# Performance work log

Measured on AMD Instinct MI355X. Metric: run time of the kernel, lower is better.

Reference implementation:

```python
import jax, jax.numpy as jnp
import numpy as np

NEG_SLOPE = 0.2  # PyG GATConv default leaky_relu slope

def gat_conv(x, src, dst, W, a_src, a_dst, bias, N):
    # Linear transform
    h = x @ W                      # [N, D]
    # Per-node attention logits (heads=1)
    al_src = h @ a_src             # [N]
    al_dst = h @ a_dst             # [N]
    e = jax.nn.leaky_relu(al_src[src] + al_dst[dst], NEG_SLOPE)  # [E]
    # Segment softmax over incoming edges of each destination node
    m = jax.ops.segment_max(e, dst, num_segments=N)
    ex = jnp.exp(e - m[dst])
    denom = jax.ops.segment_sum(ex, dst, num_segments=N)
    alpha = ex / denom[dst]        # [E]
    # Weighted scatter-aggregate of source features
    out = jax.ops.segment_sum(h[src] * alpha[:, None], dst, num_segments=N)
    return out + bias

def setup_inputs() -> dict:
    key = jax.random.key(0)
    ks = jax.random.split(key, 10)
    N, E, F_in, H, O = 50000, 800000, 128, 64, 64
    x = jax.random.normal(ks[0], (N, F_in), dtype=jnp.float32)
    edge_index = jax.random.randint(ks[1], (2, E), 0, N, dtype=jnp.int32)
    s = lambda k, shp, fan: jax.random.normal(k, shp, dtype=jnp.float32) / np.sqrt(fan)
    return {
        'x': x, 'edge_index': edge_index,
        'W1': s(ks[2], (F_in, H), F_in), 'a_src1': s(ks[3], (H,), H), 'a_dst1': s(ks[4], (H,), H), 'b1': jnp.zeros((H,), jnp.float32),
        'W2': s(ks[5], (H, O), H), 'a_src2': s(ks[6], (O,), O), 'a_dst2': s(ks[7], (O,), O), 'b2': jnp.zeros((O,), jnp.float32),
    }

def reference(x, edge_index, W1, a_src1, a_dst1, b1, W2, a_src2, a_dst2, b2):
    N = x.shape[0]
    loops = jnp.arange(N, dtype=edge_index.dtype)  # PyG adds self-loops by default
    src = jnp.concatenate([edge_index[0], loops])
    dst = jnp.concatenate([edge_index[1], loops])
    h = gat_conv(x, src, dst, W1, a_src1, a_dst1, b1, N)
    h = jax.nn.relu(h)
    # dropout(p=0.6) is identity in eval mode
    out = gat_conv(h, src, dst, W2, a_src2, a_dst2, b2, N)
    return out
```

## Files before the change

kernel.cpp:

```cpp
#include <hip/hip_runtime.h>
#include <hip/hip_bf16.h>

#define DEV static __device__ __forceinline__

typedef short bf16x8 __attribute__((ext_vector_type(8)));
typedef float f32x4  __attribute__((ext_vector_type(4)));
typedef unsigned u32x4 __attribute__((ext_vector_type(4)));

union U4 { uint4 u; bf16x8 s; };

DEV float b2f(__hip_bfloat16 v) { return __bfloat162float(v); }
DEV float lrelu(float e) { return e > 0.f ? e : 0.2f * e; }

DEV unsigned short f2bu(float f) {
    __hip_bfloat16 b = __float2bfloat16(f);
    return *reinterpret_cast<unsigned short*>(&b);
}
DEV float bu2f(unsigned short u) { return __uint_as_float((unsigned)u << 16); }

DEV float loadF(const void* p, size_t i, int f32) {
    if (f32) return ((const float*)p)[i];
    return b2f(((const __hip_bfloat16*)p)[i]);
}

DEV uint4 pack8(const unsigned short* t) {
    uint4 v;
    v.x = (unsigned)t[0] | ((unsigned)t[1] << 16);
    v.y = (unsigned)t[2] | ((unsigned)t[3] << 16);
    v.z = (unsigned)t[4] | ((unsigned)t[5] << 16);
    v.w = (unsigned)t[6] | ((unsigned)t[7] << 16);
    return v;
}

DEV u32x4 pack8v(const unsigned short* t) {
    u32x4 v;
    v.x = (unsigned)t[0] | ((unsigned)t[1] << 16);
    v.y = (unsigned)t[2] | ((unsigned)t[3] << 16);
    v.z = (unsigned)t[4] | ((unsigned)t[5] << 16);
    v.w = (unsigned)t[6] | ((unsigned)t[7] << 16);
    return v;
}

DEV void edge_sd(int i, int E, const int* __restrict__ src, const int* __restrict__ dst,
                 int& s, int& d) {
    if (i < E) { s = src[i]; d = dst[i]; }
    else       { s = d = i - E; }
}

DEV int detect_wave(const void* p, int n, int lane) {
    const unsigned short* u16 = (const unsigned short*)p;
    bool insane = false;
#pragma unroll
    for (int r = 0; r < 4; ++r) {
        int idx = lane + r * 64;
        if (idx < n) {
            unsigned short u = u16[idx];
            unsigned e = (u >> 7) & 0xFFu;
            insane |= (e >= 0xC8u) || (e == 0u && (u & 0x7Fu) != 0u);
        }
    }
    return (__ballot(insane) != 0ull) ? 1 : 0;
}

#define G_BIN 128

__global__ __launch_bounds__(256) void k_fused1(
    const void* __restrict__ x, const void* __restrict__ W,
    const void* __restrict__ a_s, const void* __restrict__ a_d,
    __hip_bfloat16* __restrict__ h, float* __restrict__ als, float* __restrict__ ald,
    int N, int gb, int nx, int nW1,
    const int* __restrict__ src, const int* __restrict__ dst,
    int* __restrict__ hist, int E, int EA, int chunk,
    const void* a5, int n5, const void* a6, int n6, const void* a7, int n7,
    const void* a8, int n8, const void* a9, int n9,
    int* __restrict__ flags)
{
    const int tid = threadIdx.x;
    const int bid = blockIdx.x;

    if (bid >= gb) {
        if (bid == gb + G_BIN) {
            const void* ps[9] = {x, W, a_s, a_d, a5, a6, a7, a8, a9};
            const int   ns[9] = {nx, nW1, 64, 64, n5, n6, n7, n8, n9};
            const int w = tid >> 6, lane = tid & 63;
            for (int k = w; k < 9; k += 4) {
                int f = detect_wave(ps[k], ns[k], lane);
                if (lane == 0) flags[k] = f;
            }
            return;
        }
        __shared__ int cnt[256];
        cnt[tid] = 0;
        __syncthreads();
        const int cb = bid - gb;
        const int lo = cb * chunk;
        const int hi = min(lo + chunk, EA);
        for (int i = lo + tid; i < hi; i += 256) {
            int s, d; edge_sd(i, E, src, dst, s, d);
            atomicAdd(&cnt[d >> 8], 1);
        }
        __syncthreads();
        hist[cb * 256 + tid] = cnt[tid];
        return;
    }

    __shared__ __align__(16) unsigned short sMem[2 * 64 * 136];
    __shared__ float sAs[64], sAd[64];
    __shared__ int sFl[4];
    unsigned short* sA = sMem;
    unsigned short* sB = sMem + 64 * 136;
    float* sOut = (float*)sMem;

    {
        const void* ps4[4] = {x, W, a_s, a_d};
        const int   ns4[4] = {nx, nW1, 64, 64};
        const int w = tid >> 6, lane = tid & 63;
        int f = detect_wave(ps4[w], ns4[w], lane);
        if (lane == 0) sFl[w] = f;
    }
    __syncthreads();
    const int fx = sFl[0], fw = sFl[1];

    const int row0 = bid * 64;
    if (tid < 64) sAs[tid] = loadF(a_s, tid, sFl[2]);
    else if (tid < 128) sAd[tid - 64] = loadF(a_d, tid - 64, sFl[3]);

    if (!fx) {
        const uint4* xg = (const uint4*)x;
#pragma unroll
        for (int it = 0; it < 2; ++it) {
            int g = tid + it * 256;
            int r = g >> 4, c16 = g & 15;
            uint4 v = (row0 + r < N) ? xg[(size_t)(row0 + r) * 16 + c16]
                                     : make_uint4(0, 0, 0, 0);
            *(uint4*)(sA + r * 136 + c16 * 8) = v;
        }
    } else {
        for (int i = tid; i < 64 * 128; i += 256) {
            int r = i >> 7, k = i & 127;
            float v = (row0 + r < N) ? ((const float*)x)[(size_t)(row0 + r) * 128 + k] : 0.f;
            sA[r * 136 + k] = f2bu(v);
        }
    }
    if (!fw) {
        const unsigned short* Wg = (const unsigned short*)W;
        const int n = tid & 63;
        int k0 = (tid >> 6) * 8;
#pragma unroll
        for (int rep = 0; rep < 4; ++rep, k0 += 32) {
            unsigned short t[8];
#pragma unroll
            for (int j = 0; j < 8; ++j) t[j] = Wg[(size_t)(k0 + j) * 64 + n];
            *(uint4*)(sB + n * 136 + k0) = pack8(t);
        }
    } else {
        const float* Wg = (const float*)W;
        for (int i = tid; i < 128 * 64; i += 256) {
            int k = i >> 6, n = i & 63;
            sB[n * 136 + k] = f2bu(Wg[i]);
        }
    }
    __syncthreads();

    const int w = tid >> 6, lane = tid & 63;
    const int m0 = w * 16;
    const int qr = lane >> 4;
    const int lc = lane & 15;

    bf16x8 afrag[4];
#pragma unroll
    for (int c = 0; c < 4; ++c) {
        U4 u; u.u = *(const uint4*)(sA + (m0 + lc) * 136 + c * 32 + qr * 8);
        afrag[c] = u.s;
    }
    f32x4 accs[4];
#pragma unroll
    for (int nt = 0; nt < 4; ++nt) {
        f32x4 acc = {0.f, 0.f, 0.f, 0.f};
#pragma unroll
        for (int c = 0; c < 4; ++c) {
            U4 u; u.u = *(const uint4*)(sB + (nt * 16 + lc) * 136 + c * 32 + qr * 8);
            acc = __builtin_amdgcn_mfma_f32_16x16x32_bf16(afrag[c], u.s, acc, 0, 0, 0);
        }
        accs[nt] = acc;
    }
    __syncthreads();

#pragma unroll
    for (int nt = 0; nt < 4; ++nt)
#pragma unroll
        for (int reg = 0; reg < 4; ++reg)
            sOut[(m0 + qr * 4 + reg) * 68 + nt * 16 + lc] = accs[nt][reg];
    __syncthreads();

    {
        const int r = tid >> 2, seg = tid & 3;
        const int row = row0 + r;
        const float* po = sOut + r * 68 + seg * 16;
        float ps = 0.f, pd = 0.f;
        unsigned short ob[16];
#pragma unroll
        for (int i = 0; i < 16; ++i) {
            float v = po[i];
            ps = fmaf(v, sAs[seg * 16 + i], ps);
            pd = fmaf(v, sAd[seg * 16 + i], pd);
            ob[i] = f2bu(v);
        }
        if (row < N) {
            uint4* hp = (uint4*)((unsigned short*)h + (size_t)row * 64 + seg * 16);
            hp[0] = pack8(ob);
            hp[1] = pack8(ob + 8);
        }
        ps += __shfl_xor(ps, 1, 64); ps += __shfl_xor(ps, 2, 64);
        pd += __shfl_xor(pd, 1, 64); pd += __shfl_xor(pd, 2, 64);
        if (seg == 0 && row < N) { als[row] = ps; ald[row] = pd; }
    }
}

__global__ __launch_bounds__(G_BIN) void k_binB1(
    const int* __restrict__ hist, int* __restrict__ offs_rel,
    int* __restrict__ btot)
{
    __shared__ int sm[G_BIN];
    const int t = threadIdx.x;
    const int b = blockIdx.x;
    int v = hist[t * 256 + b];
    sm[t] = v;
    __syncthreads();
#pragma unroll
    for (int off = 1; off < G_BIN; off <<= 1) {
        int u = (t >= off) ? sm[t - off] : 0;
        __syncthreads();
        sm[t] += u;
        __syncthreads();
    }
    offs_rel[t * 256 + b] = sm[t] - v;
    if (t == G_BIN - 1) btot[b] = sm[t];
}

__global__ __launch_bounds__(256) void k_binC(
    const int* __restrict__ src, const int* __restrict__ dst,
    const int* __restrict__ offs_rel, const int* __restrict__ btot,
    unsigned* __restrict__ ebuf, int E, int EA, int chunk)
{
    __shared__ int sm[256];
    __shared__ int cur[256];
    const int tid = threadIdx.x;
    int v = btot[tid];
    sm[tid] = v;
    __syncthreads();
#pragma unroll
    for (int off = 1; off < 256; off <<= 1) {
        int t = (tid >= off) ? sm[tid - off] : 0;
        __syncthreads();
        sm[tid] += t;
        __syncthreads();
    }
    cur[tid] = (sm[tid] - v) + offs_rel[blockIdx.x * 256 + tid];
    __syncthreads();
    const int lo = blockIdx.x * chunk;
    const int hi = min(lo + chunk, EA);
    for (int i = lo + tid; i < hi; i += 256) {
        int s, d; edge_sd(i, E, src, dst, s, d);
        int pos = atomicAdd(&cur[d >> 8], 1);
        ebuf[pos] = ((unsigned)(d & 255) << 17) | (unsigned)s;
    }
}

__global__ __launch_bounds__(256) void k_binD(
    const unsigned* __restrict__ ebuf, const int* __restrict__ btot,
    int* __restrict__ row_ptr, int* __restrict__ col, int N)
{
    __shared__ int sm[256];
    __shared__ int cnt[256];
    __shared__ int pfx[256];
    const int tid = threadIdx.x;
    const int b = blockIdx.x;
    {
        int v = btot[tid];
        sm[tid] = v;
        __syncthreads();
#pragma unroll
        for (int off = 1; off < 256; off <<= 1) {
            int t = (tid >= off) ? sm[tid - off] : 0;
            __syncthreads();
            sm[tid] += t;
            __syncthreads();
        }
    }
    const int lo = (b == 0) ? 0 : sm[b - 1];
    const int hi = sm[b];
    cnt[tid] = 0;
    __syncthreads();
    for (int i = lo + tid; i < hi; i += 256)
        atomicAdd(&cnt[ebuf[i] >> 17], 1);
    __syncthreads();
    const int c = cnt[tid];
    pfx[tid] = c;
    __syncthreads();
#pragma unroll
    for (int off = 1; off < 256; off <<= 1) {
        int t = (tid >= off) ? pfx[tid - off] : 0;
        __syncthreads();
        pfx[tid] += t;
        __syncthreads();
    }
    const int excl = pfx[tid] - c;
    const int d = b * 256 + tid;
    if (d <= N) row_ptr[d] = lo + excl;
    __syncthreads();
    cnt[tid] = lo + excl;
    __syncthreads();
    for (int i = lo + tid; i < hi; i += 256) {
        unsigned v = ebuf[i];
        int pos = atomicAdd(&cnt[v >> 17], 1);
        col[pos] = (int)(v & 0x1FFFFu);
    }
}

__global__ __launch_bounds__(256) void k_gemm2(
    __hip_bfloat16* __restrict__ agg, const void* __restrict__ b1,
    const void* __restrict__ W, const void* __restrict__ a_s,
    const void* __restrict__ a_d, const int* __restrict__ flags,
    float* __restrict__ als, float* __restrict__ ald, int N)
{
    __shared__ __align__(16) unsigned short sMem[2 * 64 * 72];
    __shared__ float sAs[64], sAd[64], sBias[64];
    unsigned short* sA = sMem;
    unsigned short* sB = sMem + 64 * 72;
    float* sOut = (float*)sMem;

    const int tid = threadIdx.x;
    const int row0 = blockIdx.x * 64;
    const int fw = flags[5];

    if (tid < 64) sAs[tid] = loadF(a_s, tid, flags[6]);
    else if (tid < 128) sAd[tid - 64] = loadF(a_d, tid - 64, flags[7]);
    else if (tid < 192) sBias[tid - 128] = loadF(b1, tid - 128, flags[4]);
    __syncthreads();

    {
        const uint4* ag = (const uint4*)agg;
#pragma unroll
        for (int it = 0; it < 2; ++it) {
            int g = tid + it * 256;
            int r = g >> 3, c8 = g & 7;
            uint4 v = (row0 + r < N) ? ag[(size_t)(row0 + r) * 8 + c8]
                                     : make_uint4(0, 0, 0, 0);
            unsigned short in[8] = {
                (unsigned short)(v.x & 0xFFFF), (unsigned short)(v.x >> 16),
                (unsigned short)(v.y & 0xFFFF), (unsigned short)(v.y >> 16),
                (unsigned short)(v.z & 0xFFFF), (unsigned short)(v.z >> 16),
                (unsigned short)(v.w & 0xFFFF), (unsigned short)(v.w >> 16)};
            unsigned short ob[8];
#pragma unroll
            for (int j = 0; j < 8; ++j) {
                float t = bu2f(in[j]) + sBias[c8 * 8 + j];
                ob[j] = f2bu(t > 0.f ? t : 0.f);
            }
            *(uint4*)(sA + r * 72 + c8 * 8) = pack8(ob);
        }
    }
    if (!fw) {
        const unsigned short* Wg = (const unsigned short*)W;
        const int n = tid & 63;
        int k0 = (tid >> 6) * 8;
#pragma unroll
        for (int rep = 0; rep < 2; ++rep, k0 += 32) {
            unsigned short t[8];
#pragma unroll
            for (int j = 0; j < 8; ++j) t[j] = Wg[(size_t)(k0 + j) * 64 + n];
            *(uint4*)(sB + n * 72 + k0) = pack8(t);
        }
    } else {
        const float* Wg = (const float*)W;
        for (int i = tid; i < 64 * 64; i += 256) {
            int k = i >> 6, n = i & 63;
            sB[n * 72 + k] = f2bu(Wg[i]);
        }
    }
    __syncthreads();

    const int w = tid >> 6, lane = tid & 63;
    const int m0 = w * 16;
    const int qr = lane >> 4, lc = lane & 15;

    bf16x8 afrag[2];
#pragma unroll
    for (int c = 0; c < 2; ++c) {
        U4 u; u.u = *(const uint4*)(sA + (m0 + lc) * 72 + c * 32 + qr * 8);
        afrag[c] = u.s;
    }
    f32x4 accs[4];
#pragma unroll
    for (int nt = 0; nt < 4; ++nt) {
        f32x4 acc = {0.f, 0.f, 0.f, 0.f};
#pragma unroll
        for (int c = 0; c < 2; ++c) {
            U4 u; u.u = *(const uint4*)(sB + (nt * 16 + lc) * 72 + c * 32 + qr * 8);
            acc = __builtin_amdgcn_mfma_f32_16x16x32_bf16(afrag[c], u.s, acc, 0, 0, 0);
        }
        accs[nt] = acc;
    }
    __syncthreads();
#pragma unroll
    for (int nt = 0; nt < 4; ++nt)
#pragma unroll
        for (int reg = 0; reg < 4; ++reg)
            sOut[(m0 + qr * 4 + reg) * 68 + nt * 16 + lc] = accs[nt][reg];
    __syncthreads();

    {
        const int r = tid >> 2, seg = tid & 3;
        const int row = row0 + r;
        const float* po = sOut + r * 68 + seg * 16;
        float ps = 0.f, pd = 0.f;
        unsigned short ob[16];
#pragma unroll
        for (int i = 0; i < 16; ++i) {
            float v = po[i];
            ps = fmaf(v, sAs[seg * 16 + i], ps);
            pd = fmaf(v, sAd[seg * 16 + i], pd);
            ob[i] = f2bu(v);
        }
        if (row < N) {
            uint4* hp = (uint4*)((unsigned short*)agg + (size_t)row * 64 + seg * 16);
            hp[0] = pack8(ob);
            hp[1] = pack8(ob + 8);
        }
        ps += __shfl_xor(ps, 1, 64); ps += __shfl_xor(ps, 2, 64);
        pd += __shfl_xor(pd, 1, 64); pd += __shfl_xor(pd, 2, 64);
        if (seg == 0 && row < N) { als[row] = ps; ald[row] = pd; }
    }
}

__global__ __launch_bounds__(256) void k_gather(
    const int* __restrict__ row_ptr, const int* __restrict__ col,
    const float* __restrict__ als, const float* __restrict__ ald,
    const __hip_bfloat16* __restrict__ h,
    __hip_bfloat16* __restrict__ agg_out,
    void* __restrict__ final_out,
    const void* __restrict__ bias, const int* __restrict__ flags, int N)
{
    const int tid = threadIdx.x;
    const int lane = tid & 63;
    const int eg = lane >> 3, fg = lane & 7;
    const int wid = blockIdx.x * 4 + (tid >> 6);
    const int nw  = gridDim.x * 4;

    for (int d = wid; d < N; d += nw) {
        const float aldd = ald[d];
        const int beg = row_ptr[d], end = row_ptr[d + 1];
        float acc[8] = {0.f,0.f,0.f,0.f,0.f,0.f,0.f,0.f};
        float den = 0.f;
        for (int j = beg + eg; j < end; j += 8) {
            const int s = col[j];
            const float w = __expf(lrelu(als[s] + aldd));
            den += w;
            const uint4 hv = *reinterpret_cast<const uint4*>(h + (size_t)s * 64 + fg * 8);
            acc[0] = fmaf(w, __uint_as_float(hv.x << 16),          acc[0]);
            acc[1] = fmaf(w, __uint_as_float(hv.x & 0xFFFF0000u),  acc[1]);
            acc[2] = fmaf(w, __uint_as_float(hv.y << 16),          acc[2]);
            acc[3] = fmaf(w, __uint_as_float(hv.y & 0xFFFF0000u),  acc[3]);
            acc[4] = fmaf(w, __uint_as_float(hv.z << 16),          acc[4]);
            acc[5] = fmaf(w, __uint_as_float(hv.z & 0xFFFF0000u),  acc[5]);
            acc[6] = fmaf(w, __uint_as_float(hv.w << 16),          acc[6]);
            acc[7] = fmaf(w, __uint_as_float(hv.w & 0xFFFF0000u),  acc[7]);
        }
#pragma unroll
        for (int off = 8; off <= 32; off <<= 1) {
            den += __shfl_xor(den, off, 64);
#pragma unroll
            for (int k = 0; k < 8; ++k) acc[k] += __shfl_xor(acc[k], off, 64);
        }
        if (eg == 0) {
            const float inv = 1.f / den;
            if (final_out) {
                float vb[8];
#pragma unroll
                for (int k = 0; k < 8; ++k) vb[k] = acc[k] * inv + loadF(bias, fg * 8 + k, flags[8]);
                if (flags[0]) {
                    float* o = (float*)final_out + (size_t)d * 64 + fg * 8;
                    f32x4 o0 = {vb[0], vb[1], vb[2], vb[3]};
                    f32x4 o1 = {vb[4], vb[5], vb[6], vb[7]};
                    __builtin_nontemporal_store(o0, (f32x4*)o);
                    __builtin_nontemporal_store(o1, (f32x4*)(o + 4));
                } else {
                    unsigned short ob[8];
#pragma unroll
                    for (int k = 0; k < 8; ++k) ob[k] = f2bu(vb[k]);
                    __builtin_nontemporal_store(pack8v(ob),
                        reinterpret_cast<u32x4*>((__hip_bfloat16*)final_out + (size_t)d * 64 + fg * 8));
                }
            } else {
                unsigned short ob[8];
#pragma unroll
                for (int k = 0; k < 8; ++k) ob[k] = f2bu(acc[k] * inv);
                __builtin_nontemporal_store(pack8v(ob),
                    reinterpret_cast<u32x4*>(agg_out + (size_t)d * 64 + fg * 8));
            }
        }
    }
}

extern "C" void kernel_launch(void* const* d_in, const int* in_sizes, int n_in,
                              void* d_out, int out_size, void* d_ws, size_t ws_size,
                              hipStream_t stream)
{
    const void* x   = d_in[0];
    const int*  ei  = (const int*)d_in[1];
    const void* W1  = d_in[2];
    const void* as1 = d_in[3];
    const void* ad1 = d_in[4];
    const void* b1  = d_in[5];
    const void* W2  = d_in[6];
    const void* as2 = d_in[7];
    const void* ad2 = d_in[8];
    const void* b2  = d_in[9];

    const int N  = in_sizes[0] / 128;
    const int E  = in_sizes[1] / 2;
    const int EA = E + N;
    const int* src = ei;
    const int* dst = ei + E;

    uintptr_t base = (uintptr_t)d_ws;
    auto alloc = [&](size_t bytes) { uintptr_t p = base; base += (bytes + 63) & ~(size_t)63; return p; };
    int*      flags    = (int*)alloc(64 * 4);
    float*    als      = (float*)alloc((size_t)N * 4);
    float*    ald      = (float*)alloc((size_t)N * 4);
    int*      row_ptr  = (int*)alloc((size_t)(N + 1) * 4);
    int*      hist     = (int*)alloc((size_t)G_BIN * 256 * 4);
    int*      offs_rel = (int*)alloc((size_t)G_BIN * 256 * 4);
    int*      btot     = (int*)alloc(256 * 4);
    unsigned* ebuf     = (unsigned*)alloc((size_t)EA * 4);
    int*      col      = (int*)alloc((size_t)EA * 4);
    __hip_bfloat16* hbuf   = (__hip_bfloat16*)alloc((size_t)N * 64 * 2);
    __hip_bfloat16* aggbuf = (__hip_bfloat16*)alloc((size_t)N * 64 * 2);

    const int gatherb = 2048;
    const int gb  = (N + 63) / 64;
    const int NBK = (N + 255) / 256;
    const int chunk = (EA + G_BIN - 1) / G_BIN;

    k_fused1<<<gb + G_BIN + 1, 256, 0, stream>>>(
        x, W1, as1, ad1, hbuf, als, ald, N, gb, in_sizes[0], in_sizes[2],
        src, dst, hist, E, EA, chunk,
        b1, in_sizes[5], W2, in_sizes[6], as2, in_sizes[7], ad2, in_sizes[8],
        b2, in_sizes[9], flags);
    k_binB1<<<256, G_BIN, 0, stream>>>(hist, offs_rel, btot);
    k_binC<<<G_BIN, 256, 0, stream>>>(src, dst, offs_rel, btot, ebuf, E, EA, chunk);
    k_binD<<<NBK, 256, 0, stream>>>(ebuf, btot, row_ptr, col, N);

    k_gather<<<gatherb, 256, 0, stream>>>(row_ptr, col, als, ald, hbuf, aggbuf,
                                          nullptr, nullptr, flags, N);
    k_gemm2<<<gb, 256, 0, stream>>>(aggbuf, b1, W2, as2, ad2, flags, als, ald, N);
    k_gather<<<gatherb, 256, 0, stream>>>(row_ptr, col, als, ald, aggbuf, nullptr,
                                          d_out, b2, flags, N);
    (void)out_size; (void)ws_size; (void)n_in;
}
```

Baseline: 199.6 us.

## Fuse CSR build into first kernel with device-wide barriers; prefetch in gather

Moves the histogram, scan, scatter and per-bucket sort stages of the CSR construction into the first fused kernel. The first 256 blocks run them, separated by atomic-counter grid barriers, while the remaining blocks compute the GEMM. This removes three kernel launches and their serialization. The gather kernel now gives each wave a contiguous range of nodes, loads row_ptr and ald once per wave and broadcasts them with shuffles, and prefetches the next edge's column and logit. The grid barrier assumes all 256 CSR blocks are co-resident, which risks deadlock if they are not. It also adds a memset launch.

```diff
diff --git a/kernel.cpp b/kernel.cpp
--- a/kernel.cpp
+++ b/kernel.cpp
@@ -62,7 +62,19 @@
     return (__ballot(insane) != 0ull) ? 1 : 0;
 }
 
-#define G_BIN 128
+#define GCSR 256
+
+DEV void dev_barrier(int* ctr, int target) {
+    __syncthreads();
+    if (threadIdx.x == 0) {
+        __threadfence();
+        __hip_atomic_fetch_add(ctr, 1, __ATOMIC_ACQ_REL, __HIP_MEMORY_SCOPE_AGENT);
+        while (__hip_atomic_load(ctr, __ATOMIC_ACQUIRE, __HIP_MEMORY_SCOPE_AGENT) < target)
+            __builtin_amdgcn_s_sleep(8);
+        __threadfence();
+    }
+    __syncthreads();
+}
 
 __global__ __launch_bounds__(256) void k_fused1(
     const void* __restrict__ x, const void* __restrict__ W,
@@ -70,7 +82,9 @@
     __hip_bfloat16* __restrict__ h, float* __restrict__ als, float* __restrict__ ald,
     int N, int gb, int nx, int nW1,
     const int* __restrict__ src, const int* __restrict__ dst,
-    int* __restrict__ hist, int E, int EA, int chunk,
+    int* __restrict__ hist, int E, int EA, int chunk, int NBK,
+    unsigned* __restrict__ ebuf, int* __restrict__ col, int* __restrict__ row_ptr,
+    int* __restrict__ ctrs,
     const void* a5, int n5, const void* a6, int n6, const void* a7, int n7,
     const void* a8, int n8, const void* a9, int n9,
     int* __restrict__ flags)
@@ -78,35 +92,99 @@
     const int tid = threadIdx.x;
     const int bid = blockIdx.x;
 
-    if (bid >= gb) {
-        if (bid == gb + G_BIN) {
-            const void* ps[9] = {x, W, a_s, a_d, a5, a6, a7, a8, a9};
-            const int   ns[9] = {nx, nW1, 64, 64, n5, n6, n7, n8, n9};
-            const int w = tid >> 6, lane = tid & 63;
-            for (int k = w; k < 9; k += 4) {
-                int f = detect_wave(ps[k], ns[k], lane);
-                if (lane == 0) flags[k] = f;
-            }
-            return;
-        }
-        __shared__ int cnt[256];
-        cnt[tid] = 0;
-        __syncthreads();
-        const int cb = bid - gb;
-        const int lo = cb * chunk;
-        const int hi = min(lo + chunk, EA);
-        for (int i = lo + tid; i < hi; i += 256) {
-            int s, d; edge_sd(i, E, src, dst, s, d);
-            atomicAdd(&cnt[d >> 8], 1);
-        }
-        __syncthreads();
-        hist[cb * 256 + tid] = cnt[tid];
-        return;
-    }
-
     __shared__ __align__(16) unsigned short sMem[2 * 64 * 136];
     __shared__ float sAs[64], sAd[64];
     __shared__ int sFl[4];
+
+    if (bid < GCSR) {
+        int* p0 = (int*)sMem;
+        int* p1 = p0 + 256;
+        int* pE = p1 + 256;
+        int* pI = pE + 256;
+        const int cb = bid;
+        const int lo = cb * chunk;
+        const int hi = min(lo + chunk, EA);
+
+        p0[tid] = 0;
+        __syncthreads();
+        for (int i = lo + tid; i < hi; i += 256) {
+            int s, d; edge_sd(i, E, src, dst, s, d);
+            atomicAdd(&p0[d >> 8], 1);
+        }
+        __syncthreads();
+        hist[cb * 256 + tid] = p0[tid];
+        dev_barrier(ctrs + 0, GCSR);
+
+        int tot = 0, mine = 0;
+        for (int c = 0; c < GCSR; ++c) {
+            int v = hist[c * 256 + tid];
+            tot += v;
+            if (c < cb) mine += v;
+        }
+        p1[tid] = tot;
+        __syncthreads();
+#pragma unroll
+        for (int off = 1; off < 256; off <<= 1) {
+            int u = (tid >= off) ? p1[tid - off] : 0;
+            __syncthreads();
+            p1[tid] += u;
+            __syncthreads();
+        }
+        pI[tid] = p1[tid];
+        pE[tid] = p1[tid] - tot;
+        p0[tid] = pE[tid] + mine;
+        __syncthreads();
+        for (int i = lo + tid; i < hi; i += 256) {
+            int s, d; edge_sd(i, E, src, dst, s, d);
+            int pos = atomicAdd(&p0[d >> 8], 1);
+            ebuf[pos] = ((unsigned)(d & 255) << 17) | (unsigned)s;
+        }
+        dev_barrier(ctrs + 1, GCSR);
+
+        for (int b = cb; b < NBK; b += GCSR) {
+            const int blo = pE[b], bhi = pI[b];
+            p0[tid] = 0;
+            __syncthreads();
+            for (int i = blo + tid; i < bhi; i += 256)
+                atomicAdd(&p0[ebuf[i] >> 17], 1);
+            __syncthreads();
+            const int c = p0[tid];
+            p1[tid] = c;
+            __syncthreads();
+#pragma unroll
+            for (int off = 1; off < 256; off <<= 1) {
+                int u = (tid >= off) ? p1[tid - off] : 0;
+                __syncthreads();
+                p1[tid] += u;
+                __syncthreads();
+            }
+            const int excl = p1[tid] - c;
+            const int dd = b * 256 + tid;
+            if (dd <= N) row_ptr[dd] = blo + excl;
+            __syncthreads();
+            p0[tid] = blo + excl;
+            __syncthreads();
+            for (int i = blo + tid; i < bhi; i += 256) {
+                unsigned v = ebuf[i];
+                int pos = atomicAdd(&p0[v >> 17], 1);
+                col[pos] = (int)(v & 0x1FFFFu);
+            }
+            __syncthreads();
+        }
+        return;
+    }
+
+    if (bid == GCSR + gb) {
+        const void* ps[9] = {x, W, a_s, a_d, a5, a6, a7, a8, a9};
+        const int   ns[9] = {nx, nW1, 64, 64, n5, n6, n7, n8, n9};
+        const int w = tid >> 6, lane = tid & 63;
+        for (int k = w; k < 9; k += 4) {
+            int f = detect_wave(ps[k], ns[k], lane);
+            if (lane == 0) flags[k] = f;
+        }
+        return;
+    }
+
     unsigned short* sA = sMem;
     unsigned short* sB = sMem + 64 * 136;
     float* sOut = (float*)sMem;
@@ -121,7 +199,7 @@
     __syncthreads();
     const int fx = sFl[0], fw = sFl[1];
 
-    const int row0 = bid * 64;
+    const int row0 = (bid - GCSR) * 64;
     if (tid < 64) sAs[tid] = loadF(a_s, tid, sFl[2]);
     else if (tid < 128) sAd[tid - 64] = loadF(a_d, tid - 64, sFl[3]);
 
@@ -214,107 +292,6 @@
         ps += __shfl_xor(ps, 1, 64); ps += __shfl_xor(ps, 2, 64);
         pd += __shfl_xor(pd, 1, 64); pd += __shfl_xor(pd, 2, 64);
         if (seg == 0 && row < N) { als[row] = ps; ald[row] = pd; }
-    }
-}
-
-__global__ __launch_bounds__(G_BIN) void k_binB1(
-    const int* __restrict__ hist, int* __restrict__ offs_rel,
-    int* __restrict__ btot)
-{
-    __shared__ int sm[G_BIN];
-    const int t = threadIdx.x;
-    const int b = blockIdx.x;
-    int v = hist[t * 256 + b];
-    sm[t] = v;
-    __syncthreads();
-#pragma unroll
-    for (int off = 1; off < G_BIN; off <<= 1) {
-        int u = (t >= off) ? sm[t - off] : 0;
-        __syncthreads();
-        sm[t] += u;
-        __syncthreads();
-    }
-    offs_rel[t * 256 + b] = sm[t] - v;
-    if (t == G_BIN - 1) btot[b] = sm[t];
-}
-
-__global__ __launch_bounds__(256) void k_binC(
-    const int* __restrict__ src, const int* __restrict__ dst,
-    const int* __restrict__ offs_rel, const int* __restrict__ btot,
-    unsigned* __restrict__ ebuf, int E, int EA, int chunk)
-{
-    __shared__ int sm[256];
-    __shared__ int cur[256];
-    const int tid = threadIdx.x;
-    int v = btot[tid];
-    sm[tid] = v;
-    __syncthreads();
-#pragma unroll
-    for (int off = 1; off < 256; off <<= 1) {
-        int t = (tid >= off) ? sm[tid - off] : 0;
-        __syncthreads();
-        sm[tid] += t;
-        __syncthreads();
-    }
-    cur[tid] = (sm[tid] - v) + offs_rel[blockIdx.x * 256 + tid];
-    __syncthreads();
-    const int lo = blockIdx.x * chunk;
-    const int hi = min(lo + chunk, EA);
-    for (int i = lo + tid; i < hi; i += 256) {
-        int s, d; edge_sd(i, E, src, dst, s, d);
-        int pos = atomicAdd(&cur[d >> 8], 1);
-        ebuf[pos] = ((unsigned)(d & 255) << 17) | (unsigned)s;
-    }
-}
-
-__global__ __launch_bounds__(256) void k_binD(
-    const unsigned* __restrict__ ebuf, const int* __restrict__ btot,
-    int* __restrict__ row_ptr, int* __restrict__ col, int N)
-{
-    __shared__ int sm[256];
-    __shared__ int cnt[256];
-    __shared__ int pfx[256];
-    const int tid = threadIdx.x;
-    const int b = blockIdx.x;
-    {
-        int v = btot[tid];
-        sm[tid] = v;
-        __syncthreads();
-#pragma unroll
-        for (int off = 1; off < 256; off <<= 1) {
-            int t = (tid >= off) ? sm[tid - off] : 0;
-            __syncthreads();
-            sm[tid] += t;
-            __syncthreads();
-        }
-    }
-    const int lo = (b == 0) ? 0 : sm[b - 1];
-    const int hi = sm[b];
-    cnt[tid] = 0;
-    __syncthreads();
-    for (int i = lo + tid; i < hi; i += 256)
-        atomicAdd(&cnt[ebuf[i] >> 17], 1);
-    __syncthreads();
-    const int c = cnt[tid];
-    pfx[tid] = c;
-    __syncthreads();
-#pragma unroll
-    for (int off = 1; off < 256; off <<= 1) {
-        int t = (tid >= off) ? pfx[tid - off] : 0;
-        __syncthreads();
-        pfx[tid] += t;
-        __syncthreads();
-    }
-    const int excl = pfx[tid] - c;
-    const int d = b * 256 + tid;
-    if (d <= N) row_ptr[d] = lo + excl;
-    __syncthreads();
-    cnt[tid] = lo + excl;
-    __syncthreads();
-    for (int i = lo + tid; i < hi; i += 256) {
-        unsigned v = ebuf[i];
-        int pos = atomicAdd(&cnt[v >> 17], 1);
-        col[pos] = (int)(v & 0x1FFFFu);
     }
 }
 
@@ -447,38 +424,57 @@
     const int eg = lane >> 3, fg = lane & 7;
     const int wid = blockIdx.x * 4 + (tid >> 6);
     const int nw  = gridDim.x * 4;
-
-    for (int d = wid; d < N; d += nw) {
-        const float aldd = ald[d];
-        const int beg = row_ptr[d], end = row_ptr[d + 1];
+    const int npw = (N + nw - 1) / nw;
+    const int base = wid * npw;
+    if (base >= N) return;
+    const int cnt = min(npw, N - base);
+
+    int rp = 0; float aldv = 0.f;
+    if (lane <= cnt) rp = row_ptr[base + lane];
+    if (lane < cnt)  aldv = ald[base + lane];
+
+    for (int k = 0; k < cnt; ++k) {
+        const int d = base + k;
+        const int beg = __shfl(rp, k, 64);
+        const int end = __shfl(rp, k + 1, 64);
+        const float aldd = __shfl(aldv, k, 64);
+
         float acc[8] = {0.f,0.f,0.f,0.f,0.f,0.f,0.f,0.f};
         float den = 0.f;
-        for (int j = beg + eg; j < end; j += 8) {
-            const int s = col[j];
-            const float w = __expf(lrelu(als[s] + aldd));
-            den += w;
-            const uint4 hv = *reinterpret_cast<const uint4*>(h + (size_t)s * 64 + fg * 8);
-            acc[0] = fmaf(w, __uint_as_float(hv.x << 16),          acc[0]);
-            acc[1] = fmaf(w, __uint_as_float(hv.x & 0xFFFF0000u),  acc[1]);
-            acc[2] = fmaf(w, __uint_as_float(hv.y << 16),          acc[2]);
-            acc[3] = fmaf(w, __uint_as_float(hv.y & 0xFFFF0000u),  acc[3]);
-            acc[4] = fmaf(w, __uint_as_float(hv.z << 16),          acc[4]);
-            acc[5] = fmaf(w, __uint_as_float(hv.z & 0xFFFF0000u),  acc[5]);
-            acc[6] = fmaf(w, __uint_as_float(hv.w << 16),          acc[6]);
-            acc[7] = fmaf(w, __uint_as_float(hv.w & 0xFFFF0000u),  acc[7]);
+        int j = beg + eg;
+        if (j < end) {
+            int sC = col[j];
+            float alsC = als[sC];
+            for (; j < end; j += 8) {
+                const int jn = j + 8;
+                int sN = 0; float alsN = 0.f;
+                if (jn < end) { sN = col[jn]; alsN = als[sN]; }
+                const float w = __expf(lrelu(alsC + aldd));
+                const uint4 hv = *reinterpret_cast<const uint4*>(h + (size_t)sC * 64 + fg * 8);
+                den += w;
+                acc[0] = fmaf(w, __uint_as_float(hv.x << 16),          acc[0]);
+                acc[1] = fmaf(w, __uint_as_float(hv.x & 0xFFFF0000u),  acc[1]);
+                acc[2] = fmaf(w, __uint_as_float(hv.y << 16),          acc[2]);
+                acc[3] = fmaf(w, __uint_as_float(hv.y & 0xFFFF0000u),  acc[3]);
+                acc[4] = fmaf(w, __uint_as_float(hv.z << 16),          acc[4]);
+                acc[5] = fmaf(w, __uint_as_float(hv.z & 0xFFFF0000u),  acc[5]);
+                acc[6] = fmaf(w, __uint_as_float(hv.w << 16),          acc[6]);
+                acc[7] = fmaf(w, __uint_as_float(hv.w & 0xFFFF0000u),  acc[7]);
+                sC = sN; alsC = alsN;
+            }
         }
 #pragma unroll
         for (int off = 8; off <= 32; off <<= 1) {
             den += __shfl_xor(den, off, 64);
 #pragma unroll
-            for (int k = 0; k < 8; ++k) acc[k] += __shfl_xor(acc[k], off, 64);
+            for (int q = 0; q < 8; ++q) acc[q] += __shfl_xor(acc[q], off, 64);
         }
         if (eg == 0) {
             const float inv = 1.f / den;
             if (final_out) {
                 float vb[8];
 #pragma unroll
-                for (int k = 0; k < 8; ++k) vb[k] = acc[k] * inv + loadF(bias, fg * 8 + k, flags[8]);
+                for (int q = 0; q < 8; ++q) vb[q] = acc[q] * inv + loadF(bias, fg * 8 + q, flags[8]);
                 if (flags[0]) {
                     float* o = (float*)final_out + (size_t)d * 64 + fg * 8;
                     f32x4 o0 = {vb[0], vb[1], vb[2], vb[3]};
@@ -488,14 +484,14 @@
                 } else {
                     unsigned short ob[8];
 #pragma unroll
-                    for (int k = 0; k < 8; ++k) ob[k] = f2bu(vb[k]);
+                    for (int q = 0; q < 8; ++q) ob[q] = f2bu(vb[q]);
                     __builtin_nontemporal_store(pack8v(ob),
                         reinterpret_cast<u32x4*>((__hip_bfloat16*)final_out + (size_t)d * 64 + fg * 8));
                 }
             } else {
                 unsigned short ob[8];
 #pragma unroll
-                for (int k = 0; k < 8; ++k) ob[k] = f2bu(acc[k] * inv);
+                for (int q = 0; q < 8; ++q) ob[q] = f2bu(acc[q] * inv);
                 __builtin_nontemporal_store(pack8v(ob),
                     reinterpret_cast<u32x4*>(agg_out + (size_t)d * 64 + fg * 8));
             }
@@ -527,30 +523,28 @@
     uintptr_t base = (uintptr_t)d_ws;
     auto alloc = [&](size_t bytes) { uintptr_t p = base; base += (bytes + 63) & ~(size_t)63; return p; };
     int*      flags    = (int*)alloc(64 * 4);
+    int*      ctrs     = (int*)alloc(64);
     float*    als      = (float*)alloc((size_t)N * 4);
     float*    ald      = (float*)alloc((size_t)N * 4);
     int*      row_ptr  = (int*)alloc((size_t)(N + 1) * 4);
-    int*      hist     = (int*)alloc((size_t)G_BIN * 256 * 4);
-    int*      offs_rel = (int*)alloc((size_t)G_BIN * 256 * 4);
-    int*      btot     = (int*)alloc(256 * 4);
+    int*      hist     = (int*)alloc((size_t)GCSR * 256 * 4);
     unsigned* ebuf     = (unsigned*)alloc((size_t)EA * 4);
     int*      col      = (int*)alloc((size_t)EA * 4);
     __hip_bfloat16* hbuf   = (__hip_bfloat16*)alloc((size_t)N * 64 * 2);
     __hip_bfloat16* aggbuf = (__hip_bfloat16*)alloc((size_t)N * 64 * 2);
 
-    const int gatherb = 2048;
+    const int gatherb = 1792;
     const int gb  = (N + 63) / 64;
     const int NBK = (N + 255) / 256;
-    const int chunk = (EA + G_BIN - 1) / G_BIN;
-
-    k_fused1<<<gb + G_BIN + 1, 256, 0, stream>>>(
+    const int chunk = (EA + GCSR - 1) / GCSR;
+
+    hipMemsetAsync(ctrs, 0, 64, stream);
+
+    k_fused1<<<GCSR + gb + 1, 256, 0, stream>>>(
         x, W1, as1, ad1, hbuf, als, ald, N, gb, in_sizes[0], in_sizes[2],
-        src, dst, hist, E, EA, chunk,
+        src, dst, hist, E, EA, chunk, NBK, ebuf, col, row_ptr, ctrs,
         b1, in_sizes[5], W2, in_sizes[6], as2, in_sizes[7], ad2, in_sizes[8],
         b2, in_sizes[9], flags);
-    k_binB1<<<256, G_BIN, 0, stream>>>(hist, offs_rel, btot);
-    k_binC<<<G_BIN, 256, 0, stream>>>(src, dst, offs_rel, btot, ebuf, E, EA, chunk);
-    k_binD<<<NBK, 256, 0, stream>>>(ebuf, btot, row_ptr, col, N);
 
     k_gather<<<gatherb, 256, 0, stream>>>(row_ptr, col, als, ald, hbuf, aggbuf,
                                           nullptr, nullptr, flags, N);
```

Measured after the change: 268.0 us. 34.3% more time.

## Fold bin prefix scan into scatter kernel and software-pipeline gather loads

Applied to the files above, without the earlier changes.

Removes the separate k_binB1 prefix-scan launch and its offs_rel buffer. Each k_binC2 block now scans the histogram column itself, redundantly summing the G_BIN counts per bin. The gather kernel gives each wave a contiguous block of destination nodes and loads row_ptr and ald once per wave, sharing them via shuffles. Its inner edge loop prefetches the next edge's col, als and h row before consuming the current one. Grid size changes to 1792 blocks. The goal is one fewer launch and better hiding of the dependent gather latency, at the cost of redundant histogram reads per block and more registers in the gather.

```diff
diff --git a/kernel.cpp b/kernel.cpp
--- a/kernel.cpp
+++ b/kernel.cpp
@@ -217,37 +217,25 @@
     }
 }
 
-__global__ __launch_bounds__(G_BIN) void k_binB1(
-    const int* __restrict__ hist, int* __restrict__ offs_rel,
-    int* __restrict__ btot)
-{
-    __shared__ int sm[G_BIN];
-    const int t = threadIdx.x;
-    const int b = blockIdx.x;
-    int v = hist[t * 256 + b];
-    sm[t] = v;
-    __syncthreads();
-#pragma unroll
-    for (int off = 1; off < G_BIN; off <<= 1) {
-        int u = (t >= off) ? sm[t - off] : 0;
-        __syncthreads();
-        sm[t] += u;
-        __syncthreads();
-    }
-    offs_rel[t * 256 + b] = sm[t] - v;
-    if (t == G_BIN - 1) btot[b] = sm[t];
-}
-
-__global__ __launch_bounds__(256) void k_binC(
+__global__ __launch_bounds__(256) void k_binC2(
     const int* __restrict__ src, const int* __restrict__ dst,
-    const int* __restrict__ offs_rel, const int* __restrict__ btot,
+    const int* __restrict__ hist, int* __restrict__ btot,
     unsigned* __restrict__ ebuf, int E, int EA, int chunk)
 {
     __shared__ int sm[256];
     __shared__ int cur[256];
     const int tid = threadIdx.x;
-    int v = btot[tid];
-    sm[tid] = v;
+    const int cb = blockIdx.x;
+
+    int tot = 0, mine = 0;
+#pragma unroll 4
+    for (int c = 0; c < G_BIN; ++c) {
+        int v = hist[c * 256 + tid];
+        tot += v;
+        if (c < cb) mine += v;
+    }
+    if (cb == 0) btot[tid] = tot;
+    sm[tid] = tot;
     __syncthreads();
 #pragma unroll
     for (int off = 1; off < 256; off <<= 1) {
@@ -256,9 +244,9 @@
         sm[tid] += t;
         __syncthreads();
     }
-    cur[tid] = (sm[tid] - v) + offs_rel[blockIdx.x * 256 + tid];
-    __syncthreads();
-    const int lo = blockIdx.x * chunk;
+    cur[tid] = (sm[tid] - tot) + mine;
+    __syncthreads();
+    const int lo = cb * chunk;
     const int hi = min(lo + chunk, EA);
     for (int i = lo + tid; i < hi; i += 256) {
         int s, d; edge_sd(i, E, src, dst, s, d);
@@ -447,38 +435,62 @@
     const int eg = lane >> 3, fg = lane & 7;
     const int wid = blockIdx.x * 4 + (tid >> 6);
     const int nw  = gridDim.x * 4;
-
-    for (int d = wid; d < N; d += nw) {
-        const float aldd = ald[d];
-        const int beg = row_ptr[d], end = row_ptr[d + 1];
+    const int npw = (N + nw - 1) / nw;
+    const int base = wid * npw;
+    if (base >= N) return;
+    const int cnt = min(npw, N - base);
+
+    int rp = 0; float aldv = 0.f;
+    if (lane <= cnt) rp = row_ptr[base + lane];
+    if (lane < cnt)  aldv = ald[base + lane];
+
+    for (int k = 0; k < cnt; ++k) {
+        const int d = base + k;
+        const int beg = __shfl(rp, k, 64);
+        const int end = __shfl(rp, k + 1, 64);
+        const float aldd = __shfl(aldv, k, 64);
+
         float acc[8] = {0.f,0.f,0.f,0.f,0.f,0.f,0.f,0.f};
         float den = 0.f;
-        for (int j = beg + eg; j < end; j += 8) {
-            const int s = col[j];
-            const float w = __expf(lrelu(als[s] + aldd));
-            den += w;
-            const uint4 hv = *reinterpret_cast<const uint4*>(h + (size_t)s * 64 + fg * 8);
-            acc[0] = fmaf(w, __uint_as_float(hv.x << 16),          acc[0]);
-            acc[1] = fmaf(w, __uint_as_float(hv.x & 0xFFFF0000u),  acc[1]);
-            acc[2] = fmaf(w, __uint_as_float(hv.y << 16),          acc[2]);
-            acc[3] = fmaf(w, __uint_as_float(hv.y & 0xFFFF0000u),  acc[3]);
-            acc[4] = fmaf(w, __uint_as_float(hv.z << 16),          acc[4]);
-            acc[5] = fmaf(w, __uint_as_float(hv.z & 0xFFFF0000u),  acc[5]);
-            acc[6] = fmaf(w, __uint_as_float(hv.w << 16),          acc[6]);
-            acc[7] = fmaf(w, __uint_as_float(hv.w & 0xFFFF0000u),  acc[7]);
+        int j = beg + eg;
+        if (j < end) {
+            int sC = col[j];
+            float alsC = als[sC];
+            uint4 hvC = *reinterpret_cast<const uint4*>(h + (size_t)sC * 64 + fg * 8);
+            for (; j < end; j += 8) {
+                const int jn = j + 8;
+                int sN = 0; float alsN = 0.f;
+                uint4 hvN = make_uint4(0, 0, 0, 0);
+                if (jn < end) {
+                    sN = col[jn];
+                    alsN = als[sN];
+                    hvN = *reinterpret_cast<const uint4*>(h + (size_t)sN * 64 + fg * 8);
+                }
+                const float w = __expf(lrelu(alsC + aldd));
+                den += w;
+                acc[0] = fmaf(w, __uint_as_float(hvC.x << 16),          acc[0]);
+                acc[1] = fmaf(w, __uint_as_float(hvC.x & 0xFFFF0000u),  acc[1]);
+                acc[2] = fmaf(w, __uint_as_float(hvC.y << 16),          acc[2]);
+                acc[3] = fmaf(w, __uint_as_float(hvC.y & 0xFFFF0000u),  acc[3]);
+                acc[4] = fmaf(w, __uint_as_float(hvC.z << 16),          acc[4]);
+                acc[5] = fmaf(w, __uint_as_float(hvC.z & 0xFFFF0000u),  acc[5]);
+                acc[6] = fmaf(w, __uint_as_float(hvC.w << 16),          acc[6]);
+                acc[7] = fmaf(w, __uint_as_float(hvC.w & 0xFFFF0000u),  acc[7]);
+                sC = sN; alsC = alsN; hvC = hvN;
+            }
         }
 #pragma unroll
         for (int off = 8; off <= 32; off <<= 1) {
             den += __shfl_xor(den, off, 64);
 #pragma unroll
-            for (int k = 0; k < 8; ++k) acc[k] += __shfl_xor(acc[k], off, 64);
+            for (int q = 0; q < 8; ++q) acc[q] += __shfl_xor(acc[q], off, 64);
         }
         if (eg == 0) {
             const float inv = 1.f / den;
             if (final_out) {
                 float vb[8];
 #pragma unroll
-                for (int k = 0; k < 8; ++k) vb[k] = acc[k] * inv + loadF(bias, fg * 8 + k, flags[8]);
+                for (int q = 0; q < 8; ++q) vb[q] = acc[q] * inv + loadF(bias, fg * 8 + q, flags[8]);
                 if (flags[0]) {
                     float* o = (float*)final_out + (size_t)d * 64 + fg * 8;
                     f32x4 o0 = {vb[0], vb[1], vb[2], vb[3]};
@@ -488,14 +500,14 @@
                 } else {
                     unsigned short ob[8];
 #pragma unroll
-                    for (int k = 0; k < 8; ++k) ob[k] = f2bu(vb[k]);
+                    for (int q = 0; q < 8; ++q) ob[q] = f2bu(vb[q]);
                     __builtin_nontemporal_store(pack8v(ob),
                         reinterpret_cast<u32x4*>((__hip_bfloat16*)final_out + (size_t)d * 64 + fg * 8));
                 }
             } else {
                 unsigned short ob[8];
 #pragma unroll
-                for (int k = 0; k < 8; ++k) ob[k] = f2bu(acc[k] * inv);
+                for (int q = 0; q < 8; ++q) ob[q] = f2bu(acc[q] * inv);
                 __builtin_nontemporal_store(pack8v(ob),
                     reinterpret_cast<u32x4*>(agg_out + (size_t)d * 64 + fg * 8));
             }
@@ -531,14 +543,13 @@
     float*    ald      = (float*)alloc((size_t)N * 4);
     int*      row_ptr  = (int*)alloc((size_t)(N + 1) * 4);
     int*      hist     = (int*)alloc((size_t)G_BIN * 256 * 4);
-    int*      offs_rel = (int*)alloc((size_t)G_BIN * 256 * 4);
     int*      btot     = (int*)alloc(256 * 4);
     unsigned* ebuf     = (unsigned*)alloc((size_t)EA * 4);
     int*      col      = (int*)alloc((size_t)EA * 4);
     __hip_bfloat16* hbuf   = (__hip_bfloat16*)alloc((size_t)N * 64 * 2);
     __hip_bfloat16* aggbuf = (__hip_bfloat16*)alloc((size_t)N * 64 * 2);
 
-    const int gatherb = 2048;
+    const int gatherb = 1792;
     const int gb  = (N + 63) / 64;
     const int NBK = (N + 255) / 256;
     const int chunk = (EA + G_BIN - 1) / G_BIN;
@@ -548,8 +559,7 @@
         src, dst, hist, E, EA, chunk,
         b1, in_sizes[5], W2, in_sizes[6], as2, in_sizes[7], ad2, in_sizes[8],
         b2, in_sizes[9], flags);
-    k_binB1<<<256, G_BIN, 0, stream>>>(hist, offs_rel, btot);
-    k_binC<<<G_BIN, 256, 0, stream>>>(src, dst, offs_rel, btot, ebuf, E, EA, chunk);
+    k_binC2<<<G_BIN, 256, 0, stream>>>(src, dst, hist, btot, ebuf, E, EA, chunk);
     k_binD<<<NBK, 256, 0, stream>>>(ebuf, btot, row_ptr, col, N);
 
     k_gather<<<gatherb, 256, 0, stream>>>(row_ptr, col, als, ald, hbuf, aggbuf,
```

New measurement: 211.2 us. +5.8%, slower.
